# Kernel tuning notes

Hardware: AMD Instinct MI355X
Metric: run time of the kernel (lower is better)

The kernel has to match this reference:

```python
import jax, jax.numpy as jnp
import numpy as np

N = 8192
K = 30


def setup_inputs() -> dict:
    key = jax.random.key(0)
    k1, k2, k3 = jax.random.split(key, 3)
    estimate = jax.random.normal(k1, (N, K), dtype=jnp.float32)
    event_time = jax.random.uniform(k2, (N,), dtype=jnp.float32) * 30.0
    event = (jax.random.uniform(k3, (N,)) < 0.7).astype(jnp.float32)
    target = jnp.stack([event_time, event], axis=1)  # [N, 2]
    intervals = (jnp.arange(K, dtype=jnp.float32) + 0.5)  # midpoints per init_kwargs
    return {"estimate": estimate, "target": target, "intervals": intervals}


def reference(estimate, target, intervals):
    event_time = target[:, 0]
    event = target[:, 1] != 0
    # hazard -> survival via exclusive cumprod (pad with 1 at the front)
    hazard = jax.nn.sigmoid(estimate)                       # [N, K]
    surv = jnp.cumprod(1.0 - hazard, axis=-1)               # inclusive cumprod
    surv_prev = jnp.concatenate(
        [jnp.ones_like(surv[..., :1]), surv[..., :-1]], axis=-1
    )                                                       # S(t_{k-1}), exclusive
    pdf = hazard * surv_prev                                # [N, K]
    mrl = jnp.sum(intervals * pdf, axis=-1)                 # [N]
    # comparable pairs: i has an event and t_i < t_j
    comparable = (event_time[:, None] < event_time[None, :]) & event[:, None]
    diff = mrl[:, None] - mrl[None, :]                      # [N, N]
    cnt = jnp.sum(comparable).astype(diff.dtype)
    return jnp.sum(jnp.where(comparable, diff, 0.0)) / cnt
```

## Files before the change

kernel.cpp:

```cpp
#include <hip/hip_runtime.h>
#include <math.h>

constexpr int N = 8192;
constexpr int K = 30;
constexpr int TPB = 256;
constexpr int NI_BLOCKS = N / TPB;
constexpr int NJ_SLICES = 32;
constexpr int JSPAN = N / NJ_SLICES;
constexpr int NBLOCKS2 = NI_BLOCKS * NJ_SLICES;


__global__ void mrl_kernel(const float* __restrict__ est,
                           const float* __restrict__ intervals,
                           double* __restrict__ mrl) {
    int i = blockIdx.x * blockDim.x + threadIdx.x;
    if (i >= N) return;
    const float* e = est + (size_t)i * K;
    double sp = 1.0;
    double m  = 0.0;
#pragma unroll
    for (int k = 0; k < K; ++k) {
        double x = (double)e[k];
        double h = 1.0 / (1.0 + exp(-x));
        m += (double)intervals[k] * h * sp;
        sp *= (1.0 - h);
    }
    mrl[i] = m;
}

__global__ void __launch_bounds__(TPB, 4)
pair_kernel(const float* __restrict__ target,
            const double* __restrict__ mrl,
            double* __restrict__ partials) {
    __shared__ float  s_t[JSPAN];
    __shared__ double s_m[JSPAN];
    __shared__ double r_num[TPB];
    __shared__ double r_cnt[TPB];

    const int tid = threadIdx.x;
    const int ib  = blockIdx.x / NJ_SLICES;
    const int js  = blockIdx.x % NJ_SLICES;
    const int i   = ib * TPB + tid;
    const int j   = js * JSPAN + tid;

    const float  ti = target[2 * i];
    const bool   ei = (target[2 * i + 1] != 0.0f);
    const double mi = mrl[i];

    s_t[tid] = target[2 * j];
    s_m[tid] = mrl[j];
    __syncthreads();

    int    c0 = 0, c1 = 0, c2 = 0, c3 = 0;
    double a0 = 0.0, a1 = 0.0, a2 = 0.0, a3 = 0.0;

#pragma unroll 8
    for (int jj = 0; jj < JSPAN; jj += 4) {
        float  t0 = s_t[jj + 0], t1 = s_t[jj + 1], t2 = s_t[jj + 2], t3 = s_t[jj + 3];
        double m0 = s_m[jj + 0], m1 = s_m[jj + 1], m2 = s_m[jj + 2], m3 = s_m[jj + 3];
        bool b0 = ti < t0, b1 = ti < t1, b2 = ti < t2, b3 = ti < t3;
        c0 += b0; a0 += b0 ? m0 : 0.0;
        c1 += b1; a1 += b1 ? m1 : 0.0;
        c2 += b2; a2 += b2 ? m2 : 0.0;
        c3 += b3; a3 += b3 ? m3 : 0.0;
    }

    const int    cnt = c0 + c1 + c2 + c3;
    const double smj = (a0 + a1) + (a2 + a3);

    r_num[tid] = ei ? ((double)cnt * mi - smj) : 0.0;
    r_cnt[tid] = ei ? (double)cnt : 0.0;
    __syncthreads();
    for (int s = TPB / 2; s > 0; s >>= 1) {
        if (tid < s) {
            r_num[tid] += r_num[tid + s];
            r_cnt[tid] += r_cnt[tid + s];
        }
        __syncthreads();
    }
    if (tid == 0) {
        partials[2 * blockIdx.x]     = r_num[0];
        partials[2 * blockIdx.x + 1] = r_cnt[0];
    }
}

__global__ void final_kernel(const double* __restrict__ partials,
                             float* __restrict__ out) {
    __shared__ double r_num[TPB];
    __shared__ double r_cnt[TPB];
    const int tid = threadIdx.x;
    double n = 0.0, c = 0.0;
#pragma unroll
    for (int p = 0; p < NBLOCKS2 / TPB; ++p) {
        const int idx = p * TPB + tid;
        n += partials[2 * idx];
        c += partials[2 * idx + 1];
    }
    r_num[tid] = n;
    r_cnt[tid] = c;
    __syncthreads();
    for (int s = TPB / 2; s > 0; s >>= 1) {
        if (tid < s) {
            r_num[tid] += r_num[tid + s];
            r_cnt[tid] += r_cnt[tid + s];
        }
        __syncthreads();
    }
    if (tid == 0) out[0] = (float)(r_num[0] / r_cnt[0]);
}

extern "C" void kernel_launch(void* const* d_in, const int* in_sizes, int n_in,
                              void* d_out, int out_size, void* d_ws, size_t ws_size,
                              hipStream_t stream) {
    const float* est       = (const float*)d_in[0];
    const float* target    = (const float*)d_in[1];
    const float* intervals = (const float*)d_in[2];
    float* out = (float*)d_out;

    double* mrl      = (double*)d_ws;
    double* partials = mrl + N;

    mrl_kernel<<<NI_BLOCKS, TPB, 0, stream>>>(est, intervals, mrl);
    pair_kernel<<<NBLOCKS2, TPB, 0, stream>>>(target, mrl, partials);
    final_kernel<<<1, TPB, 0, stream>>>(partials, out);
}
```

Measured before the change: 24.44 us.

## Store MRL in fp32, split j-range finer, accumulate per-pair differences

Stores MRL values as float and computes the sigmoid with fast single-precision exp, so loads and shared memory are halved. The pair kernel now uses 64 j-slices, so each block handles only 128 j values and only some threads load tiles. Each thread accumulates the per-pair difference (mi - mj) in double instead of the count and the sum of mj, and the launch bounds are removed. The cost is reduced precision in MRL and more blocks and partials for the final reduction.

```diff
diff --git a/kernel.cpp b/kernel.cpp
--- a/kernel.cpp
+++ b/kernel.cpp
@@ -5,35 +5,34 @@
 constexpr int K = 30;
 constexpr int TPB = 256;
 constexpr int NI_BLOCKS = N / TPB;
-constexpr int NJ_SLICES = 32;
+constexpr int NJ_SLICES = 64;
 constexpr int JSPAN = N / NJ_SLICES;
 constexpr int NBLOCKS2 = NI_BLOCKS * NJ_SLICES;
 
 
 __global__ void mrl_kernel(const float* __restrict__ est,
                            const float* __restrict__ intervals,
-                           double* __restrict__ mrl) {
+                           float* __restrict__ mrl) {
     int i = blockIdx.x * blockDim.x + threadIdx.x;
     if (i >= N) return;
-    const float* e = est + (size_t)i * K;
+    const float* e = est + i * K;
     double sp = 1.0;
     double m  = 0.0;
 #pragma unroll
     for (int k = 0; k < K; ++k) {
-        double x = (double)e[k];
-        double h = 1.0 / (1.0 + exp(-x));
+        float hf = 1.0f / (1.0f + __expf(-e[k]));
+        double h = (double)hf;
         m += (double)intervals[k] * h * sp;
         sp *= (1.0 - h);
     }
-    mrl[i] = m;
+    mrl[i] = (float)m;
 }
 
-__global__ void __launch_bounds__(TPB, 4)
-pair_kernel(const float* __restrict__ target,
-            const double* __restrict__ mrl,
-            double* __restrict__ partials) {
+__global__ void pair_kernel(const float* __restrict__ target,
+                            const float* __restrict__ mrl,
+                            double* __restrict__ partials) {
     __shared__ float  s_t[JSPAN];
-    __shared__ double s_m[JSPAN];
+    __shared__ float  s_m[JSPAN];
     __shared__ double r_num[TPB];
     __shared__ double r_cnt[TPB];
 
@@ -41,35 +40,34 @@
     const int ib  = blockIdx.x / NJ_SLICES;
     const int js  = blockIdx.x % NJ_SLICES;
     const int i   = ib * TPB + tid;
-    const int j   = js * JSPAN + tid;
 
     const float  ti = target[2 * i];
     const bool   ei = (target[2 * i + 1] != 0.0f);
-    const double mi = mrl[i];
+    const double mi = (double)mrl[i];
 
-    s_t[tid] = target[2 * j];
-    s_m[tid] = mrl[j];
+    if (tid < JSPAN) {
+        const int j = js * JSPAN + tid;
+        s_t[tid] = target[2 * j];
+        s_m[tid] = mrl[j];
+    }
     __syncthreads();
 
-    int    c0 = 0, c1 = 0, c2 = 0, c3 = 0;
     double a0 = 0.0, a1 = 0.0, a2 = 0.0, a3 = 0.0;
+    int    c0 = 0,   c1 = 0,   c2 = 0,   c3 = 0;
 
 #pragma unroll 8
     for (int jj = 0; jj < JSPAN; jj += 4) {
-        float  t0 = s_t[jj + 0], t1 = s_t[jj + 1], t2 = s_t[jj + 2], t3 = s_t[jj + 3];
-        double m0 = s_m[jj + 0], m1 = s_m[jj + 1], m2 = s_m[jj + 2], m3 = s_m[jj + 3];
+        float t0 = s_t[jj + 0], t1 = s_t[jj + 1], t2 = s_t[jj + 2], t3 = s_t[jj + 3];
+        float m0 = s_m[jj + 0], m1 = s_m[jj + 1], m2 = s_m[jj + 2], m3 = s_m[jj + 3];
         bool b0 = ti < t0, b1 = ti < t1, b2 = ti < t2, b3 = ti < t3;
-        c0 += b0; a0 += b0 ? m0 : 0.0;
-        c1 += b1; a1 += b1 ? m1 : 0.0;
-        c2 += b2; a2 += b2 ? m2 : 0.0;
-        c3 += b3; a3 += b3 ? m3 : 0.0;
+        c0 += b0; a0 += b0 ? (mi - (double)m0) : 0.0;
+        c1 += b1; a1 += b1 ? (mi - (double)m1) : 0.0;
+        c2 += b2; a2 += b2 ? (mi - (double)m2) : 0.0;
+        c3 += b3; a3 += b3 ? (mi - (double)m3) : 0.0;
     }
 
-    const int    cnt = c0 + c1 + c2 + c3;
-    const double smj = (a0 + a1) + (a2 + a3);
-
-    r_num[tid] = ei ? ((double)cnt * mi - smj) : 0.0;
-    r_cnt[tid] = ei ? (double)cnt : 0.0;
+    r_num[tid] = ei ? ((a0 + a1) + (a2 + a3)) : 0.0;
+    r_cnt[tid] = ei ? (double)(c0 + c1 + c2 + c3) : 0.0;
     __syncthreads();
     for (int s = TPB / 2; s > 0; s >>= 1) {
         if (tid < s) {
@@ -117,8 +115,8 @@
     const float* intervals = (const float*)d_in[2];
     float* out = (float*)d_out;
 
-    double* mrl      = (double*)d_ws;
-    double* partials = mrl + N;
+    float*  mrl      = (float*)d_ws;
+    double* partials = (double*)((char*)d_ws + (size_t)N * sizeof(float));
 
     mrl_kernel<<<NI_BLOCKS, TPB, 0, stream>>>(est, intervals, mrl);
     pair_kernel<<<NBLOCKS2, TPB, 0, stream>>>(target, mrl, partials);
```

Result: slower. 28.91 us (+18.3%).
